# Performance work log

Measured on AMD Instinct MI355X. Metric: run time of the kernel, lower is better.

Reference implementation:

```python
import jax, jax.numpy as jnp
import numpy as np

NUM_WIRES = 4
N_LAYERS = 2
HIDDEN = 64
NUM_CLASSES = 10
B = 4096


def _ry(state, theta, wire):
    # state: (N,2,2,2,2); theta: scalar or (N,)
    st = jnp.moveaxis(state, wire + 1, 1)
    c = jnp.reshape(jnp.cos(theta / 2), (-1, 1, 1, 1))
    s = jnp.reshape(jnp.sin(theta / 2), (-1, 1, 1, 1))
    n0 = c * st[:, 0] - s * st[:, 1]
    n1 = s * st[:, 0] + c * st[:, 1]
    st = jnp.stack([n0, n1], axis=1)
    return jnp.moveaxis(st, 1, wire + 1)


def _cnot(state, ctrl, tgt):
    st = jnp.moveaxis(state, (ctrl + 1, tgt + 1), (1, 2))  # (N,2,2,2,2)
    st = jnp.stack([st[:, 0], st[:, 1, ::-1]], axis=1)
    return jnp.moveaxis(st, (1, 2), (ctrl + 1, tgt + 1))


def _zexp(state, wire):
    p = state * state  # real statevector -> probabilities
    axes = tuple(a for a in range(1, 5) if a != wire + 1)
    marg = p.sum(axes)  # (N,2)
    return marg[:, 0] - marg[:, 1]


def quantum_layer(angles, vparams):
    # angles: (N,4) data rotation angles; vparams: (2,4)
    N = angles.shape[0]
    state = jnp.zeros((N, 2, 2, 2, 2), angles.dtype).at[:, 0, 0, 0, 0].set(1.0)
    for w in range(NUM_WIRES):
        state = _ry(state, angles[:, w], w)
    for l in range(N_LAYERS):
        for w in range(NUM_WIRES):
            state = _ry(state, vparams[l, w], w)
        state = _cnot(state, 0, 1)
        state = _cnot(state, 1, 2)
        state = _cnot(state, 2, 3)
    return jnp.stack([_zexp(state, w) for w in range(NUM_WIRES)], axis=1)  # (N,4)


def setup_inputs() -> dict:
    key = jax.random.key(0)
    ks = jax.random.split(key, 8)
    x = jax.random.uniform(ks[0], (B, 28, 28), dtype=jnp.float32)
    vparams = jax.random.normal(ks[1], (N_LAYERS, NUM_WIRES), dtype=jnp.float32)
    w1 = jax.random.normal(ks[2], (HIDDEN, NUM_WIRES), dtype=jnp.float32) * 0.5
    b1 = jnp.zeros((HIDDEN,), jnp.float32)
    w2 = jax.random.normal(ks[3], (1, HIDDEN), dtype=jnp.float32) * 0.125
    b2 = jnp.zeros((1,), jnp.float32)
    W = jax.random.normal(ks[4], (NUM_CLASSES, NUM_WIRES * 14 * 14), dtype=jnp.float32) * 0.03
    b = jnp.zeros((NUM_CLASSES,), jnp.float32)
    return {"x": x, "vparams": vparams, "w1": w1, "b1": b1, "w2": w2, "b2": b2, "W": W, "b": b}


def reference(x, vparams, w1, b1, w2, b2, W, b):
    Bx = x.shape[0]
    # 2x2 stride-2 patches, order [(r,c),(r,c+1),(r+1,c),(r+1,c+1)], patches row-major
    patches = x.reshape(Bx, 14, 2, 14, 2).transpose(0, 1, 3, 2, 4).reshape(Bx, 196, 4)
    meas = quantum_layer(patches.reshape(-1, 4), vparams).reshape(Bx, 196, 4)
    h = jax.nn.relu(jnp.einsum('bpn,hn->bph', meas, w1) + b1)
    scores = (jnp.einsum('bph,oh->bpo', h, w2) + b2)[..., 0]  # (B,196)
    attn = jax.nn.softmax(scores, axis=1)[..., None]
    weighted = meas * attn
    flat = weighted.reshape(Bx, -1)  # (B,784)
    logits = flat @ W.T + b
    return jax.nn.log_softmax(logits, axis=-1)
```

## Files before the change

### kernel.cpp

```cpp
#include <hip/hip_runtime.h>
#include <math.h>

#define NP 196
#define NC 10

__global__ __launch_bounds__(256) void quanv_fused(
    const float* __restrict__ x,
    const float* __restrict__ vparams,
    const float* __restrict__ w1,
    const float* __restrict__ b1,
    const float* __restrict__ w2,
    const float* __restrict__ b2,
    const float* __restrict__ W,
    const float* __restrict__ bias,
    float* __restrict__ out)
{
    __shared__ float s_img[784];
    __shared__ float s_vc[8];
    __shared__ float s_vs[8];
    __shared__ float s_w1[256];
    __shared__ float s_b1[64];
    __shared__ float s_w2[64];
    __shared__ float s_scores[NP];
    __shared__ float s_red_max[4];
    __shared__ float s_red_sum[4];
    __shared__ float s_lred[4][NC];
    __shared__ float s_logits[NC];

    const int tid  = threadIdx.x;
    const int b    = blockIdx.x;
    const int lane = tid & 63;
    const int wv   = tid >> 6;

    if (tid < 196) {
        ((float4*)s_img)[tid] = ((const float4*)(x + (size_t)b * 784))[tid];
    }
    s_w1[tid] = w1[tid];
    if (tid < 64) { s_b1[tid] = b1[tid]; s_w2[tid] = w2[tid]; }
    if (tid < 8) {
        const float th = vparams[tid] * 0.5f;
        s_vc[tid] = __cosf(th);
        s_vs[tid] = __sinf(th);
    }
    __syncthreads();

    float meas0 = 0.f, meas1 = 0.f, meas2 = 0.f, meas3 = 0.f;
    if (tid < NP) {
        const int pr = tid / 14;
        const int pc = tid - pr * 14;
        const float2 ra = *(const float2*)(s_img + (2 * pr) * 28 + 2 * pc);
        const float2 rb = *(const float2*)(s_img + (2 * pr + 1) * 28 + 2 * pc);

        float cw[4], sw[4];
        __sincosf(ra.x * 0.5f, &sw[0], &cw[0]);
        __sincosf(ra.y * 0.5f, &sw[1], &cw[1]);
        __sincosf(rb.x * 0.5f, &sw[2], &cw[2]);
        __sincosf(rb.y * 0.5f, &sw[3], &cw[3]);

        float t[4] = {cw[0]*cw[1], cw[0]*sw[1], sw[0]*cw[1], sw[0]*sw[1]};
        float u[4] = {cw[2]*cw[3], cw[2]*sw[3], sw[2]*cw[3], sw[2]*sw[3]};
        float v[16];
        #pragma unroll
        for (int i = 0; i < 16; i++) v[i] = t[i >> 2] * u[i & 3];

        #pragma unroll
        for (int l = 0; l < 2; l++) {
            #pragma unroll
            for (int w = 0; w < 4; w++) {
                const float c = s_vc[l * 4 + w];
                const float s = s_vs[l * 4 + w];
                const int m = 8 >> w;
                #pragma unroll
                for (int i = 0; i < 16; i++) {
                    if ((i & m) == 0) {
                        const float v0 = v[i], v1 = v[i | m];
                        v[i]     = c * v0 - s * v1;
                        v[i | m] = s * v0 + c * v1;
                    }
                }
            }
            #pragma unroll
            for (int i = 0; i < 16; i++)
                if ((i & 8) && !(i & 4)) { const float tm = v[i]; v[i] = v[i | 4]; v[i | 4] = tm; }
            #pragma unroll
            for (int i = 0; i < 16; i++)
                if ((i & 4) && !(i & 2)) { const float tm = v[i]; v[i] = v[i | 2]; v[i | 2] = tm; }
            #pragma unroll
            for (int i = 0; i < 16; i++)
                if ((i & 2) && !(i & 1)) { const float tm = v[i]; v[i] = v[i | 1]; v[i | 1] = tm; }
        }

        #pragma unroll
        for (int i = 0; i < 16; i++) {
            const float p = v[i] * v[i];
            meas0 += (i & 8) ? -p : p;
            meas1 += (i & 4) ? -p : p;
            meas2 += (i & 2) ? -p : p;
            meas3 += (i & 1) ? -p : p;
        }

        float sc = b2[0];
        #pragma unroll
        for (int j = 0; j < 64; j++) {
            const float4 wj = ((const float4*)s_w1)[j];
            float h = fmaf(wj.x, meas0, fmaf(wj.y, meas1,
                      fmaf(wj.z, meas2, fmaf(wj.w, meas3, s_b1[j]))));
            h = fmaxf(h, 0.f);
            sc = fmaf(s_w2[j], h, sc);
        }
        s_scores[tid] = sc;
    }
    __syncthreads();

    const float myscore = (tid < NP) ? s_scores[tid] : -INFINITY;
    float mx = myscore;
    #pragma unroll
    for (int off = 32; off > 0; off >>= 1) mx = fmaxf(mx, __shfl_xor(mx, off));
    if (lane == 0) s_red_max[wv] = mx;
    __syncthreads();
    const float gmax = fmaxf(fmaxf(s_red_max[0], s_red_max[1]),
                             fmaxf(s_red_max[2], s_red_max[3]));
    const float e = (tid < NP) ? __expf(myscore - gmax) : 0.f;
    float sm = e;
    #pragma unroll
    for (int off = 32; off > 0; off >>= 1) sm += __shfl_xor(sm, off);
    if (lane == 0) s_red_sum[wv] = sm;
    __syncthreads();
    const float gsum = s_red_sum[0] + s_red_sum[1] + s_red_sum[2] + s_red_sum[3];
    const float attn = e / gsum;

    float acc[NC];
    #pragma unroll
    for (int o = 0; o < NC; o++) acc[o] = 0.f;
    if (tid < NP) {
        const float wm0 = attn * meas0, wm1 = attn * meas1;
        const float wm2 = attn * meas2, wm3 = attn * meas3;
        #pragma unroll
        for (int o = 0; o < NC; o++) {
            const float4 Wv = *(const float4*)(W + o * 784 + tid * 4);
            acc[o] = fmaf(wm0, Wv.x, fmaf(wm1, Wv.y, fmaf(wm2, Wv.z, wm3 * Wv.w)));
        }
    }
    #pragma unroll
    for (int o = 0; o < NC; o++) {
        float a = acc[o];
        #pragma unroll
        for (int off = 32; off > 0; off >>= 1) a += __shfl_xor(a, off);
        if (lane == 0) s_lred[wv][o] = a;
    }
    __syncthreads();
    if (tid < NC) {
        s_logits[tid] = bias[tid] + s_lred[0][tid] + s_lred[1][tid]
                      + s_lred[2][tid] + s_lred[3][tid];
    }
    __syncthreads();
    if (tid < NC) {
        float lmax = s_logits[0];
        #pragma unroll
        for (int i = 1; i < NC; i++) lmax = fmaxf(lmax, s_logits[i]);
        float lse = 0.f;
        #pragma unroll
        for (int i = 0; i < NC; i++) lse += __expf(s_logits[i] - lmax);
        out[(size_t)b * NC + tid] = s_logits[tid] - lmax - __logf(lse);
    }
}

extern "C" void kernel_launch(void* const* d_in, const int* in_sizes, int n_in,
                              void* d_out, int out_size, void* d_ws, size_t ws_size,
                              hipStream_t stream) {
    const float* x       = (const float*)d_in[0];
    const float* vparams = (const float*)d_in[1];
    const float* w1      = (const float*)d_in[2];
    const float* b1      = (const float*)d_in[3];
    const float* w2      = (const float*)d_in[4];
    const float* b2      = (const float*)d_in[5];
    const float* W       = (const float*)d_in[6];
    const float* bias    = (const float*)d_in[7];
    float* out           = (float*)d_out;

    const int B = in_sizes[0] / 784;
    quanv_fused<<<B, 256, 0, stream>>>(x, vparams, w1, b1, w2, b2, W, bias, out);
}
```

Before: 103.4 us.

## Drop LDS staging, read parameters directly, use DPP wave reductions

Removes the shared-memory staging of the image, w1/b1/w2 and the vparams cos/sin values, plus two block barriers. Each thread now loads its patch pixels from global memory, reads the MLP weights through uniform (likely scalar) loads, and computes the variational rotation sincos itself. The shuffle-based wave reductions become DPP row/broadcast steps followed by a readlane. This trades LDS traffic and barriers for redundant per-thread sincos work and uncoalesced float2 global reads of the image.

```diff
diff --git a/kernel.cpp b/kernel.cpp
--- a/kernel.cpp
+++ b/kernel.cpp
@@ -3,6 +3,36 @@
 
 #define NP 196
 #define NC 10
+
+template<int CTRL>
+__device__ __forceinline__ float dpp_sum_step(float x) {
+    int t = __builtin_amdgcn_update_dpp(0, __float_as_int(x), CTRL, 0xf, 0xf, false);
+    return x + __int_as_float(t);
+}
+template<int CTRL>
+__device__ __forceinline__ float dpp_max_step(float x) {
+    int xi = __float_as_int(x);
+    int t = __builtin_amdgcn_update_dpp(xi, xi, CTRL, 0xf, 0xf, false);
+    return fmaxf(x, __int_as_float(t));
+}
+__device__ __forceinline__ float wave_sum(float x) {
+    x = dpp_sum_step<0x111>(x);
+    x = dpp_sum_step<0x112>(x);
+    x = dpp_sum_step<0x114>(x);
+    x = dpp_sum_step<0x118>(x);
+    x = dpp_sum_step<0x142>(x);
+    x = dpp_sum_step<0x143>(x);
+    return __int_as_float(__builtin_amdgcn_readlane(__float_as_int(x), 63));
+}
+__device__ __forceinline__ float wave_max(float x) {
+    x = dpp_max_step<0x111>(x);
+    x = dpp_max_step<0x112>(x);
+    x = dpp_max_step<0x114>(x);
+    x = dpp_max_step<0x118>(x);
+    x = dpp_max_step<0x142>(x);
+    x = dpp_max_step<0x143>(x);
+    return __int_as_float(__builtin_amdgcn_readlane(__float_as_int(x), 63));
+}
 
 __global__ __launch_bounds__(256) void quanv_fused(
     const float* __restrict__ x,
@@ -15,13 +45,6 @@
     const float* __restrict__ bias,
     float* __restrict__ out)
 {
-    __shared__ float s_img[784];
-    __shared__ float s_vc[8];
-    __shared__ float s_vs[8];
-    __shared__ float s_w1[256];
-    __shared__ float s_b1[64];
-    __shared__ float s_w2[64];
-    __shared__ float s_scores[NP];
     __shared__ float s_red_max[4];
     __shared__ float s_red_sum[4];
     __shared__ float s_lred[4][NC];
@@ -32,24 +55,14 @@
     const int lane = tid & 63;
     const int wv   = tid >> 6;
 
-    if (tid < 196) {
-        ((float4*)s_img)[tid] = ((const float4*)(x + (size_t)b * 784))[tid];
-    }
-    s_w1[tid] = w1[tid];
-    if (tid < 64) { s_b1[tid] = b1[tid]; s_w2[tid] = w2[tid]; }
-    if (tid < 8) {
-        const float th = vparams[tid] * 0.5f;
-        s_vc[tid] = __cosf(th);
-        s_vs[tid] = __sinf(th);
-    }
-    __syncthreads();
-
     float meas0 = 0.f, meas1 = 0.f, meas2 = 0.f, meas3 = 0.f;
+    float myscore = -INFINITY;
     if (tid < NP) {
         const int pr = tid / 14;
         const int pc = tid - pr * 14;
-        const float2 ra = *(const float2*)(s_img + (2 * pr) * 28 + 2 * pc);
-        const float2 rb = *(const float2*)(s_img + (2 * pr + 1) * 28 + 2 * pc);
+        const float* px = x + (size_t)b * 784 + (2 * pr) * 28 + 2 * pc;
+        const float2 ra = *(const float2*)px;
+        const float2 rb = *(const float2*)(px + 28);
 
         float cw[4], sw[4];
         __sincosf(ra.x * 0.5f, &sw[0], &cw[0]);
@@ -67,8 +80,8 @@
         for (int l = 0; l < 2; l++) {
             #pragma unroll
             for (int w = 0; w < 4; w++) {
-                const float c = s_vc[l * 4 + w];
-                const float s = s_vs[l * 4 + w];
+                float c, s;
+                __sincosf(vparams[l * 4 + w] * 0.5f, &s, &c);
                 const int m = 8 >> w;
                 #pragma unroll
                 for (int i = 0; i < 16; i++) {
@@ -102,28 +115,21 @@
         float sc = b2[0];
         #pragma unroll
         for (int j = 0; j < 64; j++) {
-            const float4 wj = ((const float4*)s_w1)[j];
-            float h = fmaf(wj.x, meas0, fmaf(wj.y, meas1,
-                      fmaf(wj.z, meas2, fmaf(wj.w, meas3, s_b1[j]))));
+            float h = fmaf(w1[j * 4 + 0], meas0, fmaf(w1[j * 4 + 1], meas1,
+                      fmaf(w1[j * 4 + 2], meas2, fmaf(w1[j * 4 + 3], meas3, b1[j]))));
             h = fmaxf(h, 0.f);
-            sc = fmaf(s_w2[j], h, sc);
+            sc = fmaf(w2[j], h, sc);
         }
-        s_scores[tid] = sc;
+        myscore = sc;
     }
-    __syncthreads();
 
-    const float myscore = (tid < NP) ? s_scores[tid] : -INFINITY;
-    float mx = myscore;
-    #pragma unroll
-    for (int off = 32; off > 0; off >>= 1) mx = fmaxf(mx, __shfl_xor(mx, off));
+    float mx = wave_max(myscore);
     if (lane == 0) s_red_max[wv] = mx;
     __syncthreads();
     const float gmax = fmaxf(fmaxf(s_red_max[0], s_red_max[1]),
                              fmaxf(s_red_max[2], s_red_max[3]));
     const float e = (tid < NP) ? __expf(myscore - gmax) : 0.f;
-    float sm = e;
-    #pragma unroll
-    for (int off = 32; off > 0; off >>= 1) sm += __shfl_xor(sm, off);
+    float sm = wave_sum(e);
     if (lane == 0) s_red_sum[wv] = sm;
     __syncthreads();
     const float gsum = s_red_sum[0] + s_red_sum[1] + s_red_sum[2] + s_red_sum[3];
@@ -143,9 +149,7 @@
     }
     #pragma unroll
     for (int o = 0; o < NC; o++) {
-        float a = acc[o];
-        #pragma unroll
-        for (int off = 32; off > 0; off >>= 1) a += __shfl_xor(a, off);
+        const float a = wave_sum(acc[o]);
         if (lane == 0) s_lred[wv][o] = a;
     }
     __syncthreads();
```

New measurement: 102.5 us. About the same (-0.8%).
